# Optimization experiments

Measured on AMD Instinct MI355X. Metric: run time of the kernel, lower is better.

## Reference

```python
import jax, jax.numpy as jnp
import numpy as np
from jax import lax

N, M, D, K = 65536, 16, 128, 8
DD = D // K  # delta_d


def _normalize(x, axis):
    # torch F.normalize: x / max(||x||_2, 1e-12)
    return x / jnp.maximum(jnp.linalg.norm(x, axis=axis, keepdims=True), 1e-12)


def setup_inputs() -> dict:
    key0 = jax.random.key(0)
    k1, k2, k3, k4 = jax.random.split(key0, 4)
    h = jax.random.normal(k1, (N, D), dtype=jnp.float32)
    neighbors = jax.random.randint(k2, (N * M,), 0, N)
    stdv = 1.0 / np.sqrt(DD)
    query = jax.random.uniform(k3, (DD, DD), minval=-stdv, maxval=stdv, dtype=jnp.float32)
    key_w = jax.random.uniform(k4, (DD, DD), minval=-stdv, maxval=stdv, dtype=jnp.float32)
    return {"h": h, "neighbors": neighbors, "query": query, "key_w": key_w,
            "iterat": 3, "max_iter": 10}


def _calc_prob(x, centre, cov):
    # x: [n,1,dd], centre: [n,k,dd], cov: [n,k,dd]
    dd = centre.shape[-1]
    diff = x - centre  # [n,k,dd]
    log_result = jnp.log(cov)
    log_result = jnp.where(jnp.isnan(log_result), jnp.float32(1e-6), log_result)
    # double-log as in the original (may produce NaN for negative log_result)
    dets = jnp.exp(jnp.sum(jnp.log(log_result), axis=2))  # [n,k]
    coef = jnp.float32(1.0 / np.sqrt((2.0 * np.pi) ** dd / 2.0))
    left = coef / jnp.sqrt(dets + 1e-6)  # [n,k]
    # diff @ diag(cov) @ diff^T == sum(cov * diff^2)
    right = jnp.exp(-0.5 * jnp.sum(cov * diff * diff, axis=2))  # [n,k]
    prob = left * right
    prob = _normalize(prob, axis=1)
    prob = jnp.where(jnp.isnan(prob), jnp.float32(1e-6), prob)
    return prob


def _forward(h, neighbors, query, key_w, iterat):
    n, d = h.shape
    dd = query.shape[0]
    k = d // dd
    m = neighbors.shape[0] // n
    nb = h[neighbors].reshape(n, m, k, dd)  # neighbor gather [n,m,k,dd]
    hc = _normalize(h.reshape(n, k, dd), axis=2)  # per-capsule normalized [n,k,dd]
    q = jnp.einsum('nke,ef->nkf', hc, query)
    kk = jnp.einsum('nke,ef->nkf', hc, key_w)
    # diagonal of q @ kk^T over capsules
    att_logit = jnp.einsum('nke,nke->nk', q, kk)
    att = jax.nn.softmax(att_logit, axis=1)[..., None]  # [n,k,1]

    # ---- calcCovs (no grad in original) ----
    qs = jnp.einsum('nmke,ef->nmkf', nb, query)  # [n,m,k,dd]
    # sum over neighbors of (qs @ kk^T): [n,k,k]
    p_matrix = jnp.einsum('nmkf,njf->nkj', qs, kk)
    diagv = jnp.diagonal(p_matrix, axis1=1, axis2=2)  # [n,k]
    # torch quirk: p[i] = torch.diag(p_matrix[i]) broadcasts the diag vector across rows
    p_b = jnp.broadcast_to(diagv[:, None, :], (n, k, k))
    sub = jnp.concatenate([nb, hc[:, None]], axis=1)  # [n,m+1,k,dd]
    sub = jnp.transpose(sub, (0, 2, 1, 3))  # [n,k,m+1,dd]
    sub = _normalize(sub, axis=2)  # normalize along neighbor axis
    L = m + 1
    # torch.median returns the lower median -> sorted element at (L-1)//2
    middle = jnp.sort(sub, axis=2)[:, :, (L - 1) // 2, :]  # [n,k,dd]
    cov = jnp.einsum('nij,njd->nid', p_b, (hc - middle) ** 2)  # [n,k,dd]
    cov = lax.stop_gradient(cov)

    # ---- iterative routing ----
    ix = jnp.sum(att * hc, axis=1, keepdims=True)  # [n,1,dd]
    for _ in range(iterat):
        p = lax.stop_gradient(_calc_prob(ix, hc, cov))[..., None]  # [n,k,1]
        ix = jnp.sum(att * p * hc, axis=1, keepdims=True) / (
            jnp.sum(att * p, axis=1, keepdims=True) + 1e-9)
    x = _normalize(ix[:, 0, :], axis=1)  # [n,dd]
    return x, att[..., 0]


def reference(h, neighbors, query, key_w, iterat, max_iter):
    del max_iter  # unused in the original forward
    return _forward(h, neighbors, query, key_w, iterat)
```

## Files before the change

kernel.cpp:

```cpp
#include <hip/hip_runtime.h>
#include <hip/hip_bf16.h>

#define MD 128
#define KC 8
#define KD 16
#define MN 16
#define QS 20

static __device__ __forceinline__ float lo_bf(unsigned int w){ union{unsigned int i;float f;}c; c.i=w<<16;        return c.f; }
static __device__ __forceinline__ float hi_bf(unsigned int w){ union{unsigned int i;float f;}c; c.i=w&0xffff0000u; return c.f; }
static __device__ __forceinline__ float bf2f1(unsigned short u){ union{unsigned int i;float f;}c; c.i=((unsigned int)u)<<16; return c.f; }

template<bool BF>
static __device__ __forceinline__ float load1(const void* base, int off) {
    if (BF) return bf2f1(((const unsigned short*)base)[off]);
    return ((const float*)base)[off];
}

static __device__ __forceinline__ float fast_rsq(float x){ return __builtin_amdgcn_rsqf(x); }
static __device__ __forceinline__ float fast_rcp(float x){ return __builtin_amdgcn_rcpf(x); }

template<int CTRL>
static __device__ __forceinline__ float dpp_mov(float v) {
    return __int_as_float(__builtin_amdgcn_update_dpp(
        0, __float_as_int(v), CTRL, 0xF, 0xF, false));
}
static __device__ __forceinline__ float rsum_quad(float v) {
    v += dpp_mov<0xB1>(v);
    v += dpp_mov<0x4E>(v);
    return v;
}
static __device__ __forceinline__ float rsum_caps(float v) {
    v += __shfl_xor(v, 4);
    v += dpp_mov<0x128>(v);
    v += __shfl_xor(v, 16);
    return v;
}
static __device__ __forceinline__ float rmax_caps(float v) {
    v = fmaxf(v, __shfl_xor(v, 4));
    v = fmaxf(v, dpp_mov<0x128>(v));
    v = fmaxf(v, __shfl_xor(v, 16));
    return v;
}

static __device__ __forceinline__ void cas(float& x, float& y) {
    float lo = fminf(x, y), hi = fmaxf(x, y);
    x = lo; y = hi;
}
static __device__ __forceinline__ void sort8(float a[8]) {
    cas(a[0],a[1]); cas(a[2],a[3]); cas(a[4],a[5]); cas(a[6],a[7]);
    cas(a[0],a[2]); cas(a[1],a[3]); cas(a[4],a[6]); cas(a[5],a[7]);
    cas(a[1],a[2]); cas(a[5],a[6]);
    cas(a[0],a[4]); cas(a[2],a[6]); cas(a[2],a[4]);
    cas(a[1],a[5]); cas(a[3],a[7]); cas(a[3],a[5]);
    cas(a[1],a[2]); cas(a[3],a[4]); cas(a[5],a[6]);
}
static __device__ __forceinline__ float med17(float a[16], float self) {
    sort8(a); sort8(a + 8);
    const float* u = a; const float* v = a + 8;
    float t7 =            fminf(u[7], v[0]);
    t7 = fmaxf(t7, fminf(u[6], v[1]));
    t7 = fmaxf(t7, fminf(u[5], v[2]));
    t7 = fmaxf(t7, fminf(u[4], v[3]));
    t7 = fmaxf(t7, fminf(u[3], v[4]));
    t7 = fmaxf(t7, fminf(u[2], v[5]));
    t7 = fmaxf(t7, fminf(u[1], v[6]));
    t7 = fmaxf(t7, fminf(u[0], v[7]));
    float t8 = fmaxf(u[0], v[0]);
    t8 = fmaxf(t8, fminf(u[7], v[1]));
    t8 = fmaxf(t8, fminf(u[6], v[2]));
    t8 = fmaxf(t8, fminf(u[5], v[3]));
    t8 = fmaxf(t8, fminf(u[4], v[4]));
    t8 = fmaxf(t8, fminf(u[3], v[5]));
    t8 = fmaxf(t8, fminf(u[2], v[6]));
    t8 = fmaxf(t8, fminf(u[1], v[7]));
    return __builtin_amdgcn_fmed3f(self, t7, t8);
}

__global__ void detect_dtype(const unsigned short* __restrict__ h, int* __restrict__ flag) {
    int l = threadIdx.x;
    float m = 0.f;
    for (int i = l; i < 1024; i += 64) {
        float v = bf2f1(h[i]);
        v = (v != v) ? 1e30f : fabsf(v);
        m = fmaxf(m, v);
    }
    #pragma unroll
    for (int off = 1; off < 64; off <<= 1) m = fmaxf(m, __shfl_xor(m, off));
    if (l == 0) flag[0] = (m < 1000.0f) ? 1 : 0;
}

template<bool BF>
__global__ __launch_bounds__(256)
void attn_fwd(const void* __restrict__ hraw,
              const int* __restrict__ nbr,
              const void* __restrict__ qry,
              const void* __restrict__ keyw,
              const int* __restrict__ iterat_p,
              const int* __restrict__ flag_p,
              void* __restrict__ out,
              int n_nodes)
{
    if (flag_p[0] != (BF ? 1 : 0)) return;

    const int tid  = threadIdx.x;
    const int wid  = tid >> 6;
    const int l    = tid & 63;
    const int sub  = l & 31;
    const int half = (l >> 5) & 1;
    const int k    = sub >> 2;
    const int q4   = sub & 3;

    int n = blockIdx.x * 8 + wid * 2 + half;
    if (n >= n_nodes) n = n_nodes - 1;

    __shared__ float qry_s[16 * QS];
    __shared__ float kt_s [16 * QS];
    {
        float qv = load1<BF>(qry, tid);
        float kv = load1<BF>(keyw, tid);
        int e = tid >> 4, f = tid & 15;
        qry_s[e * QS + f] = qv;
        kt_s [f * QS + e] = kv;
    }

    int nnb = blockIdx.x * 8 + wid * 2 + ((l >> 4) & 1);
    if (nnb >= n_nodes) nnb = n_nodes - 1;
    const int nbv = nbr[nnb * MN + (l & 15)];

    float hp[4];
    if (BF) {
        const unsigned int* hw = (const unsigned int*)hraw + (size_t)n * (MD / 2);
        unsigned int w0 = hw[sub * 2], w1 = hw[sub * 2 + 1];
        hp[0] = lo_bf(w0); hp[1] = hi_bf(w0); hp[2] = lo_bf(w1); hp[3] = hi_bf(w1);
    } else {
        float4 t = ((const float4*)((const float*)hraw + (size_t)n * MD))[sub];
        hp[0] = t.x; hp[1] = t.y; hp[2] = t.z; hp[3] = t.w;
    }
    float ss = 0;
    #pragma unroll
    for (int i = 0; i < 4; ++i) ss = fmaf(hp[i], hp[i], ss);
    ss = rsum_quad(ss);
    float inv = fast_rsq(fmaxf(ss, 1e-24f));
    float hc[4];
    #pragma unroll
    for (int i = 0; i < 4; ++i) hc[i] = hp[i] * inv;

    __syncthreads();

    uint2  rb[16];
    float4 rf[16];
    const unsigned sb = (unsigned)sub * (BF ? 8u : 16u);
    #pragma unroll
    for (int m = 0; m < MN; ++m) {
        int ia = __builtin_amdgcn_readlane(nbv, m);
        int ib = __builtin_amdgcn_readlane(nbv, m + 16);
        int idx = half ? ib : ia;
        if (BF) {
            unsigned off = ((unsigned)idx << 8) + sb;
            rb[m] = *(const uint2*)((const char*)hraw + off);
        } else {
            unsigned off = ((unsigned)idx << 9) + sb;
            rf[m] = *(const float4*)((const char*)hraw + off);
        }
    }

    float hcA[4][4];
    #pragma unroll
    for (int j = 0; j < 4; ++j) {
        hcA[0][j] = dpp_mov<0x00>(hc[j]);
        hcA[1][j] = dpp_mov<0x55>(hc[j]);
        hcA[2][j] = dpp_mov<0xAA>(hc[j]);
        hcA[3][j] = dpp_mov<0xFF>(hc[j]);
    }
    float kk[4];
    #pragma unroll
    for (int i = 0; i < 4; ++i) {
        const float* row = &kt_s[(q4 * 4 + i) * QS];
        float acc = 0;
        #pragma unroll
        for (int r = 0; r < 4; ++r) {
            float4 kr = *(const float4*)(row + r * 4);
            acc = fmaf(hcA[r][0], kr.x, acc);
            acc = fmaf(hcA[r][1], kr.y, acc);
            acc = fmaf(hcA[r][2], kr.z, acc);
            acc = fmaf(hcA[r][3], kr.w, acc);
        }
        kk[i] = acc;
    }
    float kkA[4][4];
    #pragma unroll
    for (int j = 0; j < 4; ++j) {
        kkA[0][j] = dpp_mov<0x00>(kk[j]);
        kkA[1][j] = dpp_mov<0x55>(kk[j]);
        kkA[2][j] = dpp_mov<0xAA>(kk[j]);
        kkA[3][j] = dpp_mov<0xFF>(kk[j]);
    }
    float w[4];
    #pragma unroll
    for (int i = 0; i < 4; ++i) {
        const float* row = &qry_s[(q4 * 4 + i) * QS];
        float acc = 0;
        #pragma unroll
        for (int r = 0; r < 4; ++r) {
            float4 qr = *(const float4*)(row + r * 4);
            acc = fmaf(kkA[r][0], qr.x, acc);
            acc = fmaf(kkA[r][1], qr.y, acc);
            acc = fmaf(kkA[r][2], qr.z, acc);
            acc = fmaf(kkA[r][3], qr.w, acc);
        }
        w[i] = acc;
    }

    float lg = 0;
    #pragma unroll
    for (int i = 0; i < 4; ++i) lg = fmaf(hc[i], w[i], lg);
    float logit = rsum_quad(lg);
    float mx  = rmax_caps(logit);
    float ex  = __expf(logit - mx);
    float att = ex * fast_rcp(rsum_caps(ex));

    float nbs[4], mid[4];
    #pragma unroll
    for (int c = 0; c < 4; ++c) {
        float a[16];
        float sn = 0, s2 = 0;
        #pragma unroll
        for (int m = 0; m < 16; ++m) {
            float val;
            if (BF) {
                unsigned int wd = (c < 2) ? rb[m].x : rb[m].y;
                val = (c & 1) ? hi_bf(wd) : lo_bf(wd);
            } else {
                val = (c == 0) ? rf[m].x : (c == 1) ? rf[m].y : (c == 2) ? rf[m].z : rf[m].w;
            }
            a[m] = val;
            sn += val;
            s2  = fmaf(val, val, s2);
        }
        float self = hc[c];
        s2 = fmaf(self, self, s2);
        nbs[c] = sn;
        mid[c] = med17(a, self) * fast_rsq(fmaxf(s2, 1e-24f));
    }

    float dgl = 0;
    #pragma unroll
    for (int i = 0; i < 4; ++i) dgl = fmaf(nbs[i], w[i], dgl);
    float dg = rsum_quad(dgl);

    float cv[4];
    #pragma unroll
    for (int i = 0; i < 4; ++i) {
        float t = hc[i] - mid[i];
        cv[i] = rsum_caps(dg * t * t);
    }

    float lsl = 0;
    #pragma unroll
    for (int i = 0; i < 4; ++i) {
        float lr = __logf(cv[i]);
        lr = (lr != lr) ? 1e-6f : lr;
        lsl += __logf(lr);
    }
    float ls   = rsum_quad(lsl);
    float dets = __expf(ls);
    const float coef = 5.822108e-7f;
    float left = coef * fast_rsq(dets + 1e-6f);

    float ah[4], ix[4];
    #pragma unroll
    for (int i = 0; i < 4; ++i) ah[i] = att * hc[i];
    #pragma unroll
    for (int i = 0; i < 4; ++i) ix[i] = rsum_caps(ah[i]);

    const int iterat = iterat_p[0];
    for (int it = 0; it < iterat; ++it) {
        float rsl = 0;
        #pragma unroll
        for (int i = 0; i < 4; ++i) {
            float df = ix[i] - hc[i];
            rsl = fmaf(cv[i] * df, df, rsl);
        }
        float rs   = rsum_quad(rsl);
        float prob = left * __expf(-0.5f * rs);
        float p2   = rsum_caps(prob * prob);
        float pn   = prob * fast_rsq(fmaxf(p2, 1e-24f));
        pn = (pn != pn) ? 1e-6f : pn;
        float den = rsum_caps(att * pn);
        float num[4];
        #pragma unroll
        for (int i = 0; i < 4; ++i) num[i] = rsum_caps(pn * ah[i]);
        float rr = fast_rcp(den + 1e-9f);
        #pragma unroll
        for (int i = 0; i < 4; ++i) ix[i] = num[i] * rr;
    }

    float xs = 0;
    #pragma unroll
    for (int i = 0; i < 4; ++i) xs = fmaf(ix[i], ix[i], xs);
    xs = rsum_quad(xs);
    float xinv = fast_rsq(fmaxf(xs, 1e-24f));

    if (BF) {
        if (sub < 4) {
            __hip_bfloat16 b0 = __float2bfloat16(ix[0] * xinv);
            __hip_bfloat16 b1 = __float2bfloat16(ix[1] * xinv);
            __hip_bfloat16 b2 = __float2bfloat16(ix[2] * xinv);
            __hip_bfloat16 b3 = __float2bfloat16(ix[3] * xinv);
            uint2 o;
            o.x = (unsigned)(*(unsigned short*)&b0) | ((unsigned)(*(unsigned short*)&b1) << 16);
            o.y = (unsigned)(*(unsigned short*)&b2) | ((unsigned)(*(unsigned short*)&b3) << 16);
            *(uint2*)((char*)out + (size_t)n * 32 + q4 * 8) = o;
        }
        if (q4 == 0) {
            __hip_bfloat16 ba = __float2bfloat16(att);
            ((unsigned short*)out)[(size_t)n_nodes * KD + (size_t)n * KC + k] =
                *(unsigned short*)&ba;
        }
    } else {
        if (sub < 4) {
            float4 o;
            o.x = ix[0] * xinv; o.y = ix[1] * xinv; o.z = ix[2] * xinv; o.w = ix[3] * xinv;
            *(float4*)((float*)out + (size_t)n * KD + q4 * 4) = o;
        }
        if (q4 == 0) ((float*)out)[(size_t)n_nodes * KD + (size_t)n * KC + k] = att;
    }
}

extern "C" void kernel_launch(void* const* d_in, const int* in_sizes, int n_in,
                              void* d_out, int out_size, void* d_ws, size_t ws_size,
                              hipStream_t stream) {
    const void* h    = d_in[0];
    const int*  nbr  = (const int*)d_in[1];
    const void* qry  = d_in[2];
    const void* keyw = (const void*)d_in[3];
    const int*  iterat_p = (const int*)d_in[4];

    int n_nodes = in_sizes[0] / MD;
    int* flag = (int*)d_ws;

    detect_dtype<<<1, 64, 0, stream>>>((const unsigned short*)h, flag);

    int blocks = (n_nodes + 7) / 8;
    attn_fwd<true ><<<blocks, 256, 0, stream>>>(h, nbr, qry, keyw, iterat_p, flag, d_out, n_nodes);
    attn_fwd<false><<<blocks, 256, 0, stream>>>(h, nbr, qry, keyw, iterat_p, flag, d_out, n_nodes);
}
```

Before: 91.49 us.

## Use packed bf16 integer sorting for median and grid-stride the fp32 kernel

For bf16 inputs, bf16 values are mapped to order-preserving unsigned 16-bit keys, and two lanes of the median network are sorted at once with packed u16 min/max. The work for the 16-element median drops to roughly half. The kernel becomes grid-stride with per-wave shared weight tiles and no __syncthreads. The inactive fp32 variant is launched with at most 1024 blocks, which lowers the cost of blocks that exit early. The trade-off is extra key conversion work and more register pressure, and the weight matrices are reloaded on every loop iteration.

```diff
diff --git a/kernel.cpp b/kernel.cpp
--- a/kernel.cpp
+++ b/kernel.cpp
@@ -7,47 +7,69 @@
 #define MN 16
 #define QS 20
 
+typedef short          s16x2 __attribute__((ext_vector_type(2)));
+typedef unsigned short u16x2 __attribute__((ext_vector_type(2)));
+
 static __device__ __forceinline__ float lo_bf(unsigned int w){ union{unsigned int i;float f;}c; c.i=w<<16;        return c.f; }
 static __device__ __forceinline__ float hi_bf(unsigned int w){ union{unsigned int i;float f;}c; c.i=w&0xffff0000u; return c.f; }
 static __device__ __forceinline__ float bf2f1(unsigned short u){ union{unsigned int i;float f;}c; c.i=((unsigned int)u)<<16; return c.f; }
 
-template<bool BF>
-static __device__ __forceinline__ float load1(const void* base, int off) {
-    if (BF) return bf2f1(((const unsigned short*)base)[off]);
-    return ((const float*)base)[off];
-}
-
 static __device__ __forceinline__ float fast_rsq(float x){ return __builtin_amdgcn_rsqf(x); }
 static __device__ __forceinline__ float fast_rcp(float x){ return __builtin_amdgcn_rcpf(x); }
 
-template<int CTRL>
-static __device__ __forceinline__ float dpp_mov(float v) {
-    return __int_as_float(__builtin_amdgcn_update_dpp(
-        0, __float_as_int(v), CTRL, 0xF, 0xF, false));
-}
-static __device__ __forceinline__ float rsum_quad(float v) {
-    v += dpp_mov<0xB1>(v);
-    v += dpp_mov<0x4E>(v);
-    return v;
-}
-static __device__ __forceinline__ float rsum_caps(float v) {
-    v += __shfl_xor(v, 4);
-    v += dpp_mov<0x128>(v);
-    v += __shfl_xor(v, 16);
-    return v;
-}
-static __device__ __forceinline__ float rmax_caps(float v) {
-    v = fmaxf(v, __shfl_xor(v, 4));
-    v = fmaxf(v, dpp_mov<0x128>(v));
-    v = fmaxf(v, __shfl_xor(v, 16));
-    return v;
+static __device__ __forceinline__ unsigned bfkey(unsigned u) {
+    s16x2 s = __builtin_bit_cast(s16x2, u) >> 15;
+    return u ^ (__builtin_bit_cast(unsigned, s) | 0x80008000u);
+}
+static __device__ __forceinline__ unsigned bfunkey(unsigned y) {
+    s16x2 s = __builtin_bit_cast(s16x2, ~y) >> 15;
+    return y ^ (__builtin_bit_cast(unsigned, s) | 0x80008000u);
+}
+static __device__ __forceinline__ unsigned pminu(unsigned a, unsigned b) {
+    return __builtin_bit_cast(unsigned, __builtin_elementwise_min(
+        __builtin_bit_cast(u16x2, a), __builtin_bit_cast(u16x2, b)));
+}
+static __device__ __forceinline__ unsigned pmaxu(unsigned a, unsigned b) {
+    return __builtin_bit_cast(unsigned, __builtin_elementwise_max(
+        __builtin_bit_cast(u16x2, a), __builtin_bit_cast(u16x2, b)));
+}
+static __device__ __forceinline__ void pcas(unsigned& x, unsigned& y) {
+    unsigned lo = pminu(x, y), hi = pmaxu(x, y); x = lo; y = hi;
+}
+static __device__ __forceinline__ void psort8(unsigned a[8]) {
+    pcas(a[0],a[1]); pcas(a[2],a[3]); pcas(a[4],a[5]); pcas(a[6],a[7]);
+    pcas(a[0],a[2]); pcas(a[1],a[3]); pcas(a[4],a[6]); pcas(a[5],a[7]);
+    pcas(a[1],a[2]); pcas(a[5],a[6]);
+    pcas(a[0],a[4]); pcas(a[2],a[6]); pcas(a[2],a[4]);
+    pcas(a[1],a[5]); pcas(a[3],a[7]); pcas(a[3],a[5]);
+    pcas(a[1],a[2]); pcas(a[3],a[4]); pcas(a[5],a[6]);
+}
+static __device__ __forceinline__ void pmed16(unsigned a[16], unsigned& w7, unsigned& w8) {
+    psort8(a); psort8(a + 8);
+    const unsigned* u = a; const unsigned* v = a + 8;
+    unsigned t7 =             pminu(u[7], v[0]);
+    t7 = pmaxu(t7, pminu(u[6], v[1]));
+    t7 = pmaxu(t7, pminu(u[5], v[2]));
+    t7 = pmaxu(t7, pminu(u[4], v[3]));
+    t7 = pmaxu(t7, pminu(u[3], v[4]));
+    t7 = pmaxu(t7, pminu(u[2], v[5]));
+    t7 = pmaxu(t7, pminu(u[1], v[6]));
+    t7 = pmaxu(t7, pminu(u[0], v[7]));
+    unsigned t8 = pmaxu(u[0], v[0]);
+    t8 = pmaxu(t8, pminu(u[7], v[1]));
+    t8 = pmaxu(t8, pminu(u[6], v[2]));
+    t8 = pmaxu(t8, pminu(u[5], v[3]));
+    t8 = pmaxu(t8, pminu(u[4], v[4]));
+    t8 = pmaxu(t8, pminu(u[3], v[5]));
+    t8 = pmaxu(t8, pminu(u[2], v[6]));
+    t8 = pmaxu(t8, pminu(u[1], v[7]));
+    w7 = bfunkey(t7); w8 = bfunkey(t8);
 }
 
 static __device__ __forceinline__ void cas(float& x, float& y) {
-    float lo = fminf(x, y), hi = fmaxf(x, y);
-    x = lo; y = hi;
-}
-static __device__ __forceinline__ void sort8(float a[8]) {
+    float lo = fminf(x, y), hi = fmaxf(x, y); x = lo; y = hi;
+}
+static __device__ __forceinline__ void sort8f(float a[8]) {
     cas(a[0],a[1]); cas(a[2],a[3]); cas(a[4],a[5]); cas(a[6],a[7]);
     cas(a[0],a[2]); cas(a[1],a[3]); cas(a[4],a[6]); cas(a[5],a[7]);
     cas(a[1],a[2]); cas(a[5],a[6]);
@@ -55,26 +77,43 @@
     cas(a[1],a[5]); cas(a[3],a[7]); cas(a[3],a[5]);
     cas(a[1],a[2]); cas(a[3],a[4]); cas(a[5],a[6]);
 }
-static __device__ __forceinline__ float med17(float a[16], float self) {
-    sort8(a); sort8(a + 8);
+static __device__ __forceinline__ float med17f(float a[16], float self) {
+    sort8f(a); sort8f(a + 8);
     const float* u = a; const float* v = a + 8;
     float t7 =            fminf(u[7], v[0]);
-    t7 = fmaxf(t7, fminf(u[6], v[1]));
-    t7 = fmaxf(t7, fminf(u[5], v[2]));
-    t7 = fmaxf(t7, fminf(u[4], v[3]));
-    t7 = fmaxf(t7, fminf(u[3], v[4]));
-    t7 = fmaxf(t7, fminf(u[2], v[5]));
-    t7 = fmaxf(t7, fminf(u[1], v[6]));
+    t7 = fmaxf(t7, fminf(u[6], v[1])); t7 = fmaxf(t7, fminf(u[5], v[2]));
+    t7 = fmaxf(t7, fminf(u[4], v[3])); t7 = fmaxf(t7, fminf(u[3], v[4]));
+    t7 = fmaxf(t7, fminf(u[2], v[5])); t7 = fmaxf(t7, fminf(u[1], v[6]));
     t7 = fmaxf(t7, fminf(u[0], v[7]));
     float t8 = fmaxf(u[0], v[0]);
-    t8 = fmaxf(t8, fminf(u[7], v[1]));
-    t8 = fmaxf(t8, fminf(u[6], v[2]));
-    t8 = fmaxf(t8, fminf(u[5], v[3]));
-    t8 = fmaxf(t8, fminf(u[4], v[4]));
-    t8 = fmaxf(t8, fminf(u[3], v[5]));
-    t8 = fmaxf(t8, fminf(u[2], v[6]));
+    t8 = fmaxf(t8, fminf(u[7], v[1])); t8 = fmaxf(t8, fminf(u[6], v[2]));
+    t8 = fmaxf(t8, fminf(u[5], v[3])); t8 = fmaxf(t8, fminf(u[4], v[4]));
+    t8 = fmaxf(t8, fminf(u[3], v[5])); t8 = fmaxf(t8, fminf(u[2], v[6]));
     t8 = fmaxf(t8, fminf(u[1], v[7]));
     return __builtin_amdgcn_fmed3f(self, t7, t8);
+}
+
+template<int CTRL>
+static __device__ __forceinline__ float dpp_mov(float v) {
+    return __int_as_float(__builtin_amdgcn_update_dpp(
+        0, __float_as_int(v), CTRL, 0xF, 0xF, false));
+}
+static __device__ __forceinline__ float rsum_quad(float v) {
+    v += dpp_mov<0xB1>(v);
+    v += dpp_mov<0x4E>(v);
+    return v;
+}
+static __device__ __forceinline__ float rsum_caps(float v) {
+    v += __shfl_xor(v, 4);
+    v += dpp_mov<0x128>(v);
+    v += __shfl_xor(v, 16);
+    return v;
+}
+static __device__ __forceinline__ float rmax_caps(float v) {
+    v = fmaxf(v, __shfl_xor(v, 4));
+    v = fmaxf(v, dpp_mov<0x128>(v));
+    v = fmaxf(v, __shfl_xor(v, 16));
+    return v;
 }
 
 __global__ void detect_dtype(const unsigned short* __restrict__ h, int* __restrict__ flag) {
@@ -111,220 +150,234 @@
     const int k    = sub >> 2;
     const int q4   = sub & 3;
 
-    int n = blockIdx.x * 8 + wid * 2 + half;
-    if (n >= n_nodes) n = n_nodes - 1;
-
-    __shared__ float qry_s[16 * QS];
-    __shared__ float kt_s [16 * QS];
-    {
-        float qv = load1<BF>(qry, tid);
-        float kv = load1<BF>(keyw, tid);
-        int e = tid >> 4, f = tid & 15;
-        qry_s[e * QS + f] = qv;
-        kt_s [f * QS + e] = kv;
-    }
-
-    int nnb = blockIdx.x * 8 + wid * 2 + ((l >> 4) & 1);
-    if (nnb >= n_nodes) nnb = n_nodes - 1;
-    const int nbv = nbr[nnb * MN + (l & 15)];
-
-    float hp[4];
-    if (BF) {
-        const unsigned int* hw = (const unsigned int*)hraw + (size_t)n * (MD / 2);
-        unsigned int w0 = hw[sub * 2], w1 = hw[sub * 2 + 1];
-        hp[0] = lo_bf(w0); hp[1] = hi_bf(w0); hp[2] = lo_bf(w1); hp[3] = hi_bf(w1);
-    } else {
-        float4 t = ((const float4*)((const float*)hraw + (size_t)n * MD))[sub];
-        hp[0] = t.x; hp[1] = t.y; hp[2] = t.z; hp[3] = t.w;
-    }
-    float ss = 0;
-    #pragma unroll
-    for (int i = 0; i < 4; ++i) ss = fmaf(hp[i], hp[i], ss);
-    ss = rsum_quad(ss);
-    float inv = fast_rsq(fmaxf(ss, 1e-24f));
-    float hc[4];
-    #pragma unroll
-    for (int i = 0; i < 4; ++i) hc[i] = hp[i] * inv;
-
-    __syncthreads();
-
-    uint2  rb[16];
-    float4 rf[16];
-    const unsigned sb = (unsigned)sub * (BF ? 8u : 16u);
-    #pragma unroll
-    for (int m = 0; m < MN; ++m) {
-        int ia = __builtin_amdgcn_readlane(nbv, m);
-        int ib = __builtin_amdgcn_readlane(nbv, m + 16);
-        int idx = half ? ib : ia;
+    __shared__ float q_s [4][16 * QS];
+    __shared__ float kt_s[4][16 * QS];
+    float* qs  = q_s [wid];
+    float* kts = kt_s[wid];
+
+    const int iterat = iterat_p[0];
+
+    for (int base = blockIdx.x * 8; base < n_nodes; base += gridDim.x * 8) {
+        int n = base + wid * 2 + half;
+        if (n >= n_nodes) n = n_nodes - 1;
+
+        int nnb = base + wid * 2 + ((l >> 4) & 1);
+        if (nnb >= n_nodes) nnb = n_nodes - 1;
+        const int nbv = nbr[nnb * MN + (l & 15)];
+
+        uint2  hp_b; float4 hp_f;
+        if (BF) hp_b = ((const uint2*)hraw)[(size_t)n * (MD / 8) * 2 + sub];
+        else    hp_f = ((const float4*)hraw)[(size_t)n * (MD / 4) + sub];
+
+        uint2  qw_b, kw_b; float4 qw_f, kw_f;
+        if (BF) { qw_b = ((const uint2 *)qry)[l]; kw_b = ((const uint2 *)keyw)[l]; }
+        else    { qw_f = ((const float4*)qry)[l]; kw_f = ((const float4*)keyw)[l]; }
+
+        uint2  rb[16]; float4 rf[16];
+        #pragma unroll
+        for (int m = 0; m < MN; ++m) {
+            int ia  = __builtin_amdgcn_readlane(nbv, m);
+            int ib  = __builtin_amdgcn_readlane(nbv, m + 16);
+            int idx = half ? ib : ia;
+            if (BF) rb[m] = *(const uint2*) ((const char*)hraw + (((unsigned)idx << 8) + (unsigned)sub * 8u));
+            else    rf[m] = *(const float4*)((const char*)hraw + (((unsigned)idx << 9) + (unsigned)sub * 16u));
+        }
+
+        {
+            int e = l >> 2, f0 = (l & 3) * 4;
+            float4 qv, kv;
+            if (BF) {
+                qv.x = lo_bf(qw_b.x); qv.y = hi_bf(qw_b.x); qv.z = lo_bf(qw_b.y); qv.w = hi_bf(qw_b.y);
+                kv.x = lo_bf(kw_b.x); kv.y = hi_bf(kw_b.x); kv.z = lo_bf(kw_b.y); kv.w = hi_bf(kw_b.y);
+            } else { qv = qw_f; kv = kw_f; }
+            *(float4*)&qs[e * QS + f0] = qv;
+            kts[(f0 + 0) * QS + e] = kv.x;
+            kts[(f0 + 1) * QS + e] = kv.y;
+            kts[(f0 + 2) * QS + e] = kv.z;
+            kts[(f0 + 3) * QS + e] = kv.w;
+        }
+
+        float hp[4];
+        if (BF) { hp[0]=lo_bf(hp_b.x); hp[1]=hi_bf(hp_b.x); hp[2]=lo_bf(hp_b.y); hp[3]=hi_bf(hp_b.y); }
+        else    { hp[0]=hp_f.x; hp[1]=hp_f.y; hp[2]=hp_f.z; hp[3]=hp_f.w; }
+        float ss = 0;
+        #pragma unroll
+        for (int i = 0; i < 4; ++i) ss = fmaf(hp[i], hp[i], ss);
+        ss = rsum_quad(ss);
+        float inv = fast_rsq(fmaxf(ss, 1e-24f));
+        float hc[4];
+        #pragma unroll
+        for (int i = 0; i < 4; ++i) hc[i] = hp[i] * inv;
+
+        float hcA[4][4];
+        #pragma unroll
+        for (int j = 0; j < 4; ++j) {
+            hcA[0][j] = dpp_mov<0x00>(hc[j]); hcA[1][j] = dpp_mov<0x55>(hc[j]);
+            hcA[2][j] = dpp_mov<0xAA>(hc[j]); hcA[3][j] = dpp_mov<0xFF>(hc[j]);
+        }
+        float kk[4];
+        #pragma unroll
+        for (int i = 0; i < 4; ++i) {
+            const float* row = &kts[(q4 * 4 + i) * QS];
+            float acc = 0;
+            #pragma unroll
+            for (int r = 0; r < 4; ++r) {
+                float4 kr = *(const float4*)(row + r * 4);
+                acc = fmaf(hcA[r][0], kr.x, acc); acc = fmaf(hcA[r][1], kr.y, acc);
+                acc = fmaf(hcA[r][2], kr.z, acc); acc = fmaf(hcA[r][3], kr.w, acc);
+            }
+            kk[i] = acc;
+        }
+        float kkA[4][4];
+        #pragma unroll
+        for (int j = 0; j < 4; ++j) {
+            kkA[0][j] = dpp_mov<0x00>(kk[j]); kkA[1][j] = dpp_mov<0x55>(kk[j]);
+            kkA[2][j] = dpp_mov<0xAA>(kk[j]); kkA[3][j] = dpp_mov<0xFF>(kk[j]);
+        }
+        float w[4];
+        #pragma unroll
+        for (int i = 0; i < 4; ++i) {
+            const float* row = &qs[(q4 * 4 + i) * QS];
+            float acc = 0;
+            #pragma unroll
+            for (int r = 0; r < 4; ++r) {
+                float4 qr = *(const float4*)(row + r * 4);
+                acc = fmaf(kkA[r][0], qr.x, acc); acc = fmaf(kkA[r][1], qr.y, acc);
+                acc = fmaf(kkA[r][2], qr.z, acc); acc = fmaf(kkA[r][3], qr.w, acc);
+            }
+            w[i] = acc;
+        }
+
+        float lg = 0;
+        #pragma unroll
+        for (int i = 0; i < 4; ++i) lg = fmaf(hc[i], w[i], lg);
+        float logit = rsum_quad(lg);
+        float mx  = rmax_caps(logit);
+        float ex  = __expf(logit - mx);
+        float att = ex * fast_rcp(rsum_caps(ex));
+
+        float sn[4] = {0,0,0,0}, s2[4] = {0,0,0,0};
+        #pragma unroll
+        for (int m = 0; m < 16; ++m) {
+            float x0, x1, x2, x3;
+            if (BF) { x0=lo_bf(rb[m].x); x1=hi_bf(rb[m].x); x2=lo_bf(rb[m].y); x3=hi_bf(rb[m].y); }
+            else    { x0=rf[m].x; x1=rf[m].y; x2=rf[m].z; x3=rf[m].w; }
+            sn[0]+=x0; sn[1]+=x1; sn[2]+=x2; sn[3]+=x3;
+            s2[0]=fmaf(x0,x0,s2[0]); s2[1]=fmaf(x1,x1,s2[1]);
+            s2[2]=fmaf(x2,x2,s2[2]); s2[3]=fmaf(x3,x3,s2[3]);
+        }
+
+        float mid[4];
         if (BF) {
-            unsigned off = ((unsigned)idx << 8) + sb;
-            rb[m] = *(const uint2*)((const char*)hraw + off);
+            unsigned ka[16];
+            #pragma unroll
+            for (int m = 0; m < 16; ++m) ka[m] = bfkey(rb[m].x);
+            unsigned w7, w8; pmed16(ka, w7, w8);
+            mid[0] = __builtin_amdgcn_fmed3f(hc[0], lo_bf(w7), lo_bf(w8));
+            mid[1] = __builtin_amdgcn_fmed3f(hc[1], hi_bf(w7), hi_bf(w8));
+            unsigned kb[16];
+            #pragma unroll
+            for (int m = 0; m < 16; ++m) kb[m] = bfkey(rb[m].y);
+            pmed16(kb, w7, w8);
+            mid[2] = __builtin_amdgcn_fmed3f(hc[2], lo_bf(w7), lo_bf(w8));
+            mid[3] = __builtin_amdgcn_fmed3f(hc[3], hi_bf(w7), hi_bf(w8));
         } else {
-            unsigned off = ((unsigned)idx << 9) + sb;
-            rf[m] = *(const float4*)((const char*)hraw + off);
-        }
-    }
-
-    float hcA[4][4];
-    #pragma unroll
-    for (int j = 0; j < 4; ++j) {
-        hcA[0][j] = dpp_mov<0x00>(hc[j]);
-        hcA[1][j] = dpp_mov<0x55>(hc[j]);
-        hcA[2][j] = dpp_mov<0xAA>(hc[j]);
-        hcA[3][j] = dpp_mov<0xFF>(hc[j]);
-    }
-    float kk[4];
-    #pragma unroll
-    for (int i = 0; i < 4; ++i) {
-        const float* row = &kt_s[(q4 * 4 + i) * QS];
-        float acc = 0;
-        #pragma unroll
-        for (int r = 0; r < 4; ++r) {
-            float4 kr = *(const float4*)(row + r * 4);
-            acc = fmaf(hcA[r][0], kr.x, acc);
-            acc = fmaf(hcA[r][1], kr.y, acc);
-            acc = fmaf(hcA[r][2], kr.z, acc);
-            acc = fmaf(hcA[r][3], kr.w, acc);
-        }
-        kk[i] = acc;
-    }
-    float kkA[4][4];
-    #pragma unroll
-    for (int j = 0; j < 4; ++j) {
-        kkA[0][j] = dpp_mov<0x00>(kk[j]);
-        kkA[1][j] = dpp_mov<0x55>(kk[j]);
-        kkA[2][j] = dpp_mov<0xAA>(kk[j]);
-        kkA[3][j] = dpp_mov<0xFF>(kk[j]);
-    }
-    float w[4];
-    #pragma unroll
-    for (int i = 0; i < 4; ++i) {
-        const float* row = &qry_s[(q4 * 4 + i) * QS];
-        float acc = 0;
-        #pragma unroll
-        for (int r = 0; r < 4; ++r) {
-            float4 qr = *(const float4*)(row + r * 4);
-            acc = fmaf(kkA[r][0], qr.x, acc);
-            acc = fmaf(kkA[r][1], qr.y, acc);
-            acc = fmaf(kkA[r][2], qr.z, acc);
-            acc = fmaf(kkA[r][3], qr.w, acc);
-        }
-        w[i] = acc;
-    }
-
-    float lg = 0;
-    #pragma unroll
-    for (int i = 0; i < 4; ++i) lg = fmaf(hc[i], w[i], lg);
-    float logit = rsum_quad(lg);
-    float mx  = rmax_caps(logit);
-    float ex  = __expf(logit - mx);
-    float att = ex * fast_rcp(rsum_caps(ex));
-
-    float nbs[4], mid[4];
-    #pragma unroll
-    for (int c = 0; c < 4; ++c) {
-        float a[16];
-        float sn = 0, s2 = 0;
-        #pragma unroll
-        for (int m = 0; m < 16; ++m) {
-            float val;
-            if (BF) {
-                unsigned int wd = (c < 2) ? rb[m].x : rb[m].y;
-                val = (c & 1) ? hi_bf(wd) : lo_bf(wd);
-            } else {
-                val = (c == 0) ? rf[m].x : (c == 1) ? rf[m].y : (c == 2) ? rf[m].z : rf[m].w;
-            }
-            a[m] = val;
-            sn += val;
-            s2  = fmaf(val, val, s2);
-        }
-        float self = hc[c];
-        s2 = fmaf(self, self, s2);
-        nbs[c] = sn;
-        mid[c] = med17(a, self) * fast_rsq(fmaxf(s2, 1e-24f));
-    }
-
-    float dgl = 0;
-    #pragma unroll
-    for (int i = 0; i < 4; ++i) dgl = fmaf(nbs[i], w[i], dgl);
-    float dg = rsum_quad(dgl);
-
-    float cv[4];
-    #pragma unroll
-    for (int i = 0; i < 4; ++i) {
-        float t = hc[i] - mid[i];
-        cv[i] = rsum_caps(dg * t * t);
-    }
-
-    float lsl = 0;
-    #pragma unroll
-    for (int i = 0; i < 4; ++i) {
-        float lr = __logf(cv[i]);
-        lr = (lr != lr) ? 1e-6f : lr;
-        lsl += __logf(lr);
-    }
-    float ls   = rsum_quad(lsl);
-    float dets = __expf(ls);
-    const float coef = 5.822108e-7f;
-    float left = coef * fast_rsq(dets + 1e-6f);
-
-    float ah[4], ix[4];
-    #pragma unroll
-    for (int i = 0; i < 4; ++i) ah[i] = att * hc[i];
-    #pragma unroll
-    for (int i = 0; i < 4; ++i) ix[i] = rsum_caps(ah[i]);
-
-    const int iterat = iterat_p[0];
-    for (int it = 0; it < iterat; ++it) {
-        float rsl = 0;
+            #pragma unroll
+            for (int c = 0; c < 4; ++c) {
+                float a[16];
+                #pragma unroll
+                for (int m = 0; m < 16; ++m)
+                    a[m] = (c==0) ? rf[m].x : (c==1) ? rf[m].y : (c==2) ? rf[m].z : rf[m].w;
+                mid[c] = med17f(a, hc[c]);
+            }
+        }
+        #pragma unroll
+        for (int c = 0; c < 4; ++c) {
+            float t2 = fmaf(hc[c], hc[c], s2[c]);
+            mid[c] *= fast_rsq(fmaxf(t2, 1e-24f));
+        }
+
+        float dgl = 0;
+        #pragma unroll
+        for (int i = 0; i < 4; ++i) dgl = fmaf(sn[i], w[i], dgl);
+        float dg = rsum_quad(dgl);
+
+        float cv[4];
         #pragma unroll
         for (int i = 0; i < 4; ++i) {
-            float df = ix[i] - hc[i];
-            rsl = fmaf(cv[i] * df, df, rsl);
-        }
-        float rs   = rsum_quad(rsl);
-        float prob = left * __expf(-0.5f * rs);
-        float p2   = rsum_caps(prob * prob);
-        float pn   = prob * fast_rsq(fmaxf(p2, 1e-24f));
-        pn = (pn != pn) ? 1e-6f : pn;
-        float den = rsum_caps(att * pn);
-        float num[4];
-        #pragma unroll
-        for (int i = 0; i < 4; ++i) num[i] = rsum_caps(pn * ah[i]);
-        float rr = fast_rcp(den + 1e-9f);
-        #pragma unroll
-        for (int i = 0; i < 4; ++i) ix[i] = num[i] * rr;
-    }
-
-    float xs = 0;
-    #pragma unroll
-    for (int i = 0; i < 4; ++i) xs = fmaf(ix[i], ix[i], xs);
-    xs = rsum_quad(xs);
-    float xinv = fast_rsq(fmaxf(xs, 1e-24f));
-
-    if (BF) {
-        if (sub < 4) {
-            __hip_bfloat16 b0 = __float2bfloat16(ix[0] * xinv);
-            __hip_bfloat16 b1 = __float2bfloat16(ix[1] * xinv);
-            __hip_bfloat16 b2 = __float2bfloat16(ix[2] * xinv);
-            __hip_bfloat16 b3 = __float2bfloat16(ix[3] * xinv);
-            uint2 o;
-            o.x = (unsigned)(*(unsigned short*)&b0) | ((unsigned)(*(unsigned short*)&b1) << 16);
-            o.y = (unsigned)(*(unsigned short*)&b2) | ((unsigned)(*(unsigned short*)&b3) << 16);
-            *(uint2*)((char*)out + (size_t)n * 32 + q4 * 8) = o;
-        }
-        if (q4 == 0) {
-            __hip_bfloat16 ba = __float2bfloat16(att);
-            ((unsigned short*)out)[(size_t)n_nodes * KD + (size_t)n * KC + k] =
-                *(unsigned short*)&ba;
-        }
-    } else {
-        if (sub < 4) {
-            float4 o;
-            o.x = ix[0] * xinv; o.y = ix[1] * xinv; o.z = ix[2] * xinv; o.w = ix[3] * xinv;
-            *(float4*)((float*)out + (size_t)n * KD + q4 * 4) = o;
-        }
-        if (q4 == 0) ((float*)out)[(size_t)n_nodes * KD + (size_t)n * KC + k] = att;
+            float t = hc[i] - mid[i];
+            cv[i] = rsum_caps(dg * t * t);
+        }
+
+        float lsl = 0;
+        #pragma unroll
+        for (int i = 0; i < 4; ++i) {
+            float lr = __logf(cv[i]);
+            lr = (lr != lr) ? 1e-6f : lr;
+            lsl += __logf(lr);
+        }
+        float ls   = rsum_quad(lsl);
+        float dets = __expf(ls);
+        const float coef = 5.822108e-7f;
+        float left = coef * fast_rsq(dets + 1e-6f);
+
+        float ah[4], ix[4];
+        #pragma unroll
+        for (int i = 0; i < 4; ++i) ah[i] = att * hc[i];
+        #pragma unroll
+        for (int i = 0; i < 4; ++i) ix[i] = rsum_caps(ah[i]);
+
+        for (int it = 0; it < iterat; ++it) {
+            float rsl = 0;
+            #pragma unroll
+            for (int i = 0; i < 4; ++i) {
+                float df = ix[i] - hc[i];
+                rsl = fmaf(cv[i] * df, df, rsl);
+            }
+            float rs   = rsum_quad(rsl);
+            float prob = left * __expf(-0.5f * rs);
+            float p2   = rsum_caps(prob * prob);
+            float pn   = prob * fast_rsq(fmaxf(p2, 1e-24f));
+            pn = (pn != pn) ? 1e-6f : pn;
+            float den = rsum_caps(att * pn);
+            float num[4];
+            #pragma unroll
+            for (int i = 0; i < 4; ++i) num[i] = rsum_caps(pn * ah[i]);
+            float rr = fast_rcp(den + 1e-9f);
+            #pragma unroll
+            for (int i = 0; i < 4; ++i) ix[i] = num[i] * rr;
+        }
+
+        float xs = 0;
+        #pragma unroll
+        for (int i = 0; i < 4; ++i) xs = fmaf(ix[i], ix[i], xs);
+        xs = rsum_quad(xs);
+        float xinv = fast_rsq(fmaxf(xs, 1e-24f));
+
+        if (BF) {
+            if (sub < 4) {
+                __hip_bfloat16 b0 = __float2bfloat16(ix[0] * xinv);
+                __hip_bfloat16 b1 = __float2bfloat16(ix[1] * xinv);
+                __hip_bfloat16 b2 = __float2bfloat16(ix[2] * xinv);
+                __hip_bfloat16 b3 = __float2bfloat16(ix[3] * xinv);
+                uint2 o;
+                o.x = (unsigned)(*(unsigned short*)&b0) | ((unsigned)(*(unsigned short*)&b1) << 16);
+                o.y = (unsigned)(*(unsigned short*)&b2) | ((unsigned)(*(unsigned short*)&b3) << 16);
+                *(uint2*)((char*)out + (size_t)n * 32 + q4 * 8) = o;
+            }
+            if (q4 == 0) {
+                __hip_bfloat16 ba = __float2bfloat16(att);
+                ((unsigned short*)out)[(size_t)n_nodes * KD + (size_t)n * KC + k] =
+                    *(unsigned short*)&ba;
+            }
+        } else {
+            if (sub < 4) {
+                float4 o;
+                o.x = ix[0] * xinv; o.y = ix[1] * xinv; o.z = ix[2] * xinv; o.w = ix[3] * xinv;
+                *(float4*)((float*)out + (size_t)n * KD + q4 * 4) = o;
+            }
+            if (q4 == 0) ((float*)out)[(size_t)n_nodes * KD + (size_t)n * KC + k] = att;
+        }
     }
 }
 
@@ -342,7 +395,8 @@
 
     detect_dtype<<<1, 64, 0, stream>>>((const unsigned short*)h, flag);
 
-    int blocks = (n_nodes + 7) / 8;
-    attn_fwd<true ><<<blocks, 256, 0, stream>>>(h, nbr, qry, keyw, iterat_p, flag, d_out, n_nodes);
-    attn_fwd<false><<<blocks, 256, 0, stream>>>(h, nbr, qry, keyw, iterat_p, flag, d_out, n_nodes);
-}
+    int full = (n_nodes + 7) / 8;
+    int small = full < 1024 ? full : 1024;
+    attn_fwd<true ><<<full,  256, 0, stream>>>(h, nbr, qry, keyw, iterat_p, flag, d_out, n_nodes);
+    attn_fwd<false><<<small, 256, 0, stream>>>(h, nbr, qry, keyw, iterat_p, flag, d_out, n_nodes);
+}
```

Result: no change. 91.89 us (+0.4%).
